# Optimization experiments

Hardware: AMD Instinct MI355X
Metric: run time of the kernel (lower is better)

Reference implementation:

```python
import jax, jax.numpy as jnp
import numpy as np

MODEL_DIM = 1024
N_HEADS = 16
HEAD_DIM = 64  # q_dim == k_dim == v_dim


def setup_inputs() -> dict:
    key = jax.random.key(0)
    ks = jax.random.split(key, 7)
    B, S = 4, 2048
    scale = 1.0 / np.sqrt(MODEL_DIM)
    return {
        "q": jax.random.normal(ks[0], (B, S, MODEL_DIM), dtype=jnp.float32),
        "k": jax.random.normal(ks[1], (B, S, MODEL_DIM), dtype=jnp.float32),
        "v": jax.random.normal(ks[2], (B, S, MODEL_DIM), dtype=jnp.float32),
        # Linear weights stored as [out, in] like torch; no biases.
        "wq": jax.random.normal(ks[3], (N_HEADS * HEAD_DIM, MODEL_DIM), dtype=jnp.float32) * scale,
        "wk": jax.random.normal(ks[4], (N_HEADS * HEAD_DIM, MODEL_DIM), dtype=jnp.float32) * scale,
        "wv": jax.random.normal(ks[5], (N_HEADS * HEAD_DIM, MODEL_DIM), dtype=jnp.float32) * scale,
        "wo": jax.random.normal(ks[6], (MODEL_DIM, N_HEADS * HEAD_DIM), dtype=jnp.float32) * scale,
    }


def reference(q, k, v, wq, wk, wv, wo):
    B, Sq, _ = q.shape
    Sk = k.shape[1]
    # projections: [B,S,D] @ W^T -> [B,S,H*dh] -> [B,H,S,dh]
    qh = (q @ wq.T).reshape(B, Sq, N_HEADS, HEAD_DIM).transpose(0, 2, 1, 3)
    kh = (k @ wk.T).reshape(B, Sk, N_HEADS, HEAD_DIM).transpose(0, 2, 1, 3)
    vh = (v @ wv.T).reshape(B, Sk, N_HEADS, HEAD_DIM).transpose(0, 2, 1, 3)
    # scores [B,H,Sq,Sk], scaled by sqrt(k_dim)
    scores = jnp.einsum('bhqd,bhkd->bhqk', qh, kh) / jnp.sqrt(jnp.float32(HEAD_DIM))
    attn = jax.nn.softmax(scores, axis=-1)
    ctx = jnp.einsum('bhqk,bhkd->bhqd', attn, vh)  # [B,H,Sq,dh]
    ctx = ctx.transpose(0, 2, 1, 3).reshape(B, Sq, N_HEADS * HEAD_DIM)
    return ctx @ wo.T
```

## Files before the change

### kernel.cpp

```cpp
#include <hip/hip_runtime.h>
#include <cstdint>
#include <cstddef>


typedef _Float16 f16x8 __attribute__((ext_vector_type(8)));
typedef _Float16 f16x4 __attribute__((ext_vector_type(4)));
typedef _Float16 f16x2 __attribute__((ext_vector_type(2)));
typedef __fp16 h16x2 __attribute__((ext_vector_type(2)));
typedef float f32x4 __attribute__((ext_vector_type(4)));
typedef float f32x16 __attribute__((ext_vector_type(16)));
typedef unsigned u32x4 __attribute__((ext_vector_type(4)));
typedef int i32x2 __attribute__((ext_vector_type(2)));

#define LDS_CAST(p) ((__attribute__((address_space(3))) void*)(p))
#define GLB_CAST(p) ((const __attribute__((address_space(1))) void*)(p))

__device__ __forceinline__ void gload_lds16(const void* g, void* l) {
  __builtin_amdgcn_global_load_lds(GLB_CAST(g), LDS_CAST(l), 16, 0, 0);
}

__device__ __forceinline__ float fexp2(float x) {
#if __has_builtin(__builtin_amdgcn_exp2f)
  return __builtin_amdgcn_exp2f(x);
#else
  return exp2f(x);
#endif
}

__device__ __forceinline__ f16x2 pkrtz(float a, float b) {
  h16x2 r = __builtin_amdgcn_cvt_pkrtz(a, b);
  return __builtin_bit_cast(f16x2, r);
}

__device__ __forceinline__ float dot2acc(f16x2 a, float acc) {
#if __has_builtin(__builtin_amdgcn_fdot2)
  const f16x2 one2 = {(_Float16)1.0f, (_Float16)1.0f};
  return __builtin_amdgcn_fdot2(a, one2, acc, false);
#else
  return acc + (float)a[0] + (float)a[1];
#endif
}

__device__ __forceinline__ void pl32swap(unsigned& a, unsigned& b) {
#if __has_builtin(__builtin_amdgcn_permlane32_swap)
  i32x2 r = __builtin_amdgcn_permlane32_swap((int)a, (int)b, false, false);
  a = (unsigned)r[0];
  b = (unsigned)r[1];
#else
  asm("v_permlane32_swap_b32 %0, %1" : "+v"(a), "+v"(b));
#endif
}

__global__ void cvt3_kernel(const float* __restrict__ a,
                            const float* __restrict__ b,
                            const float* __restrict__ c,
                            _Float16* __restrict__ oa, _Float16* __restrict__ ob,
                            _Float16* __restrict__ oc) {
  const float* in = blockIdx.z == 0 ? a : blockIdx.z == 1 ? b : c;
  _Float16* out = blockIdx.z == 0 ? oa : blockIdx.z == 1 ? ob : oc;
  int i = blockIdx.x * 256 + threadIdx.x;
  float4 v = ((const float4*)in)[i];
  f16x4 o = {(_Float16)v.x, (_Float16)v.y, (_Float16)v.z, (_Float16)v.w};
  ((f16x4*)out)[i] = o;
}

__global__ void cvt4_kernel(const float* __restrict__ a,
                            const float* __restrict__ b,
                            const float* __restrict__ c,
                            const float* __restrict__ d,
                            _Float16* __restrict__ oa, _Float16* __restrict__ ob,
                            _Float16* __restrict__ oc, _Float16* __restrict__ od) {
  int z = blockIdx.z;
  const float* in = z == 0 ? a : z == 1 ? b : z == 2 ? c : d;
  _Float16* out = z == 0 ? oa : z == 1 ? ob : z == 2 ? oc : od;
  int i = blockIdx.x * 256 + threadIdx.x;
  float4 v = ((const float4*)in)[i];
  f16x4 o = {(_Float16)v.x, (_Float16)v.y, (_Float16)v.z, (_Float16)v.w};
  ((f16x4*)out)[i] = o;
}

template <int MODE>
__device__ __forceinline__ void gemm_core(const _Float16* __restrict__ A,
                                          const _Float16* __restrict__ W,
                                          void* __restrict__ C, float scale,
                                          _Float16* As, _Float16* Bs) {
  constexpr int K = 1024, N = 1024;
  const int tid = threadIdx.x;
  const int wid = tid >> 6;
  const int lane = tid & 63;
  const int quad = lane >> 4;
  const int l16 = lane & 15;
  const int wm = wid >> 1;
  const int wn = wid & 1;
  const int m0 = blockIdx.y * 128;
  const int n0 = blockIdx.x * 128;

  const _Float16* Ag = A + (size_t)m0 * K;
  const _Float16* Bg = W + (size_t)n0 * K;

  f32x4 acc[4][4];
#pragma unroll
  for (int i = 0; i < 4; i++)
#pragma unroll
    for (int j = 0; j < 4; j++) acc[i][j] = (f32x4){0.f, 0.f, 0.f, 0.f};

  const int lrow = lane >> 2;
  const int lcol = (lane & 3) * 8;

  for (int k0 = 0; k0 < K; k0 += 32) {
#pragma unroll
    for (int i = 0; i < 2; i++) {
      int issue = wid * 2 + i;
      gload_lds16(Ag + (size_t)(issue * 16 + lrow) * K + k0 + lcol,
                  &As[issue * 512]);
      gload_lds16(Bg + (size_t)(issue * 16 + lrow) * K + k0 + lcol,
                  &Bs[issue * 512]);
    }
    __syncthreads();
    f16x8 af[4], bfr[4];
#pragma unroll
    for (int mt = 0; mt < 4; mt++)
      af[mt] = *(const f16x8*)&As[(wm * 64 + mt * 16 + l16) * 32 + quad * 8];
#pragma unroll
    for (int nt = 0; nt < 4; nt++)
      bfr[nt] = *(const f16x8*)&Bs[(wn * 64 + nt * 16 + l16) * 32 + quad * 8];
#pragma unroll
    for (int mt = 0; mt < 4; mt++)
#pragma unroll
      for (int nt = 0; nt < 4; nt++)
        acc[mt][nt] = __builtin_amdgcn_mfma_f32_16x16x32_f16(
            af[mt], bfr[nt], acc[mt][nt], 0, 0, 0);
    __syncthreads();
  }

#pragma unroll
  for (int mt = 0; mt < 4; mt++) {
#pragma unroll
    for (int nt = 0; nt < 4; nt++) {
#pragma unroll
      for (int r = 0; r < 4; r++) {
        int m = m0 + wm * 64 + mt * 16 + quad * 4 + r;
        int n = n0 + wn * 64 + nt * 16 + l16;
        float v = acc[mt][nt][r] * scale;
        if (MODE == 0) {
          ((float*)C)[(size_t)m * N + n] = v;
        } else {
          int b = m >> 11, s = m & 2047;
          int h = n >> 6, dd = n & 63;
          size_t bh = (size_t)(b * 16 + h);
          if (MODE == 1) {
            ((_Float16*)C)[(bh * 2048 + s) * 64 + dd] = (_Float16)v;
          } else if (MODE == 3) {
            int kt2 = s >> 5, l32k = s & 31;
            int s4 = dd >> 4, hi8 = (dd >> 3) & 1, j = dd & 7;
            size_t idx = (bh * 32 + (kt2 >> 1)) * 8192 +
                         (((kt2 & 1) * 4 + s4) * 512) + (hi8 * 32 + l32k) * 8 +
                         j;
            ((_Float16*)C)[idx] = (_Float16)v;
          } else {
            int kt = s >> 6, ks = (s >> 4) & 3, hi8 = (s >> 3) & 1, j = s & 7;
            int dt = dd >> 5, l32v = dd & 31;
            size_t idx = (bh * 32 + kt) * 8192 + 4096 + ((dt * 4 + ks) * 512) +
                         (hi8 * 32 + l32v) * 8 + j;
            ((_Float16*)C)[idx] = (_Float16)v;
          }
        }
      }
    }
  }
}

__global__ __launch_bounds__(256) void gemm_qkv(
    const _Float16* __restrict__ qb, const _Float16* __restrict__ kb,
    const _Float16* __restrict__ vb, const _Float16* __restrict__ wq,
    const _Float16* __restrict__ wk, const _Float16* __restrict__ wv,
    _Float16* __restrict__ Qh, _Float16* __restrict__ KVf) {
  __shared__ _Float16 As[128 * 32];
  __shared__ _Float16 Bs[128 * 32];
  if (blockIdx.z == 0)
    gemm_core<1>(qb, wq, Qh, 0.18033688f, As, Bs);
  else if (blockIdx.z == 1)
    gemm_core<3>(kb, wk, KVf, 1.0f, As, Bs);
  else
    gemm_core<4>(vb, wv, KVf, 1.0f, As, Bs);
}

__global__ __launch_bounds__(256) void gemm_wo(const _Float16* __restrict__ ctx,
                                               const _Float16* __restrict__ wo,
                                               float* __restrict__ out) {
  __shared__ _Float16 As[128 * 32];
  __shared__ _Float16 Bs[128 * 32];
  gemm_core<0>(ctx, wo, out, 1.0f, As, Bs);
}

__global__ __launch_bounds__(256, 3) void attn_kernel(
    const _Float16* __restrict__ Qh, const _Float16* __restrict__ KVf,
    _Float16* __restrict__ ctx) {
  __shared__ _Float16 sKV[3][8192];

  const int qt = blockIdx.x;
  const int bh = blockIdx.y;
  const int tid = threadIdx.x;
  const int wid = tid >> 6;
  const int lane = tid & 63;
  const int l32 = lane & 31;
  const int hi = lane >> 5;

  const _Float16* Qg = Qh + ((size_t)bh * 2048 + qt * 128 + wid * 32) * 64;
  const _Float16* KVb = KVf + (size_t)bh * 262144;

  f16x8 aq[4];
#pragma unroll
  for (int s = 0; s < 4; s++)
    aq[s] = *(const f16x8*)(Qg + (size_t)l32 * 64 + s * 16 + hi * 8);

  f32x16 acc[2];
#pragma unroll
  for (int i = 0; i < 16; i++) {
    acc[0][i] = 0.f;
    acc[1][i] = 0.f;
  }
  float lsA = 0.f, lsB = 0.f;

  auto stage = [&](int buf, int kt) {
    const _Float16* t = KVb + (size_t)kt * 8192;
#pragma unroll
    for (int i = 0; i < 4; i++) {
      int c = wid * 4 + i;
      gload_lds16(t + c * 512 + lane * 8, &sKV[buf][c * 512]);
    }
  };

  stage(0, 0);
  int cur = 0;

  for (int kt = 0; kt < 32; kt++) {
    int nxt = (cur == 2) ? 0 : cur + 1;
    if (kt < 31) {
      stage(nxt, kt + 1);
      asm volatile("s_waitcnt vmcnt(4)" ::: "memory");
    } else {
      asm volatile("s_waitcnt vmcnt(0)" ::: "memory");
    }
    __builtin_amdgcn_s_barrier();
    asm volatile("" ::: "memory");

    const _Float16* Ks = sKV[cur];
    const _Float16* Vs = sKV[cur] + 4096;

    f16x8 kf0[4], kf1[4];
#pragma unroll
    for (int s = 0; s < 4; s++) {
      kf0[s] = *(const f16x8*)&Ks[(0 * 4 + s) * 512 + lane * 8];
      kf1[s] = *(const f16x8*)&Ks[(4 + s) * 512 + lane * 8];
    }

    f32x16 s0, s1;
#pragma unroll
    for (int i = 0; i < 16; i++) {
      s0[i] = 0.f;
      s1[i] = 0.f;
    }
#pragma unroll
    for (int s = 0; s < 4; s++) {
      s0 = __builtin_amdgcn_mfma_f32_32x32x16_f16(kf0[s], aq[s], s0, 0, 0, 0);
      s1 = __builtin_amdgcn_mfma_f32_32x32x16_f16(kf1[s], aq[s], s1, 0, 0, 0);
    }

    f16x8 vf0[4], vf1[4];
#pragma unroll
    for (int g = 0; g < 4; g++) {
      vf0[g] = *(const f16x8*)&Vs[(0 * 4 + g) * 512 + lane * 8];
      vf1[g] = *(const f16x8*)&Vs[(4 + g) * 512 + lane * 8];
    }

    unsigned hw[2][8];
#pragma unroll
    for (int i = 0; i < 8; i++) {
      f16x2 hh = pkrtz(fexp2(s0[2 * i]), fexp2(s0[2 * i + 1]));
      if (i & 1)
        lsB = dot2acc(hh, lsB);
      else
        lsA = dot2acc(hh, lsA);
      hw[0][i] = __builtin_bit_cast(unsigned, hh);
    }
#pragma unroll
    for (int i = 0; i < 8; i++) {
      f16x2 hh = pkrtz(fexp2(s1[2 * i]), fexp2(s1[2 * i + 1]));
      if (i & 1)
        lsB = dot2acc(hh, lsB);
      else
        lsA = dot2acc(hh, lsA);
      hw[1][i] = __builtin_bit_cast(unsigned, hh);
    }

#pragma unroll
    for (int st = 0; st < 2; st++)
#pragma unroll
      for (int kh = 0; kh < 2; kh++) {
        unsigned w0 = hw[st][4 * kh + 0], w2 = hw[st][4 * kh + 2];
        unsigned w1 = hw[st][4 * kh + 1], w3 = hw[st][4 * kh + 3];
        pl32swap(w0, w2);
        pl32swap(w1, w3);
        u32x4 wv4 = {w0, w1, w2, w3};
        f16x8 pfrag = __builtin_bit_cast(f16x8, wv4);
        int g = st * 2 + kh;
        acc[0] = __builtin_amdgcn_mfma_f32_32x32x16_f16(vf0[g], pfrag, acc[0],
                                                        0, 0, 0);
        acc[1] = __builtin_amdgcn_mfma_f32_32x32x16_f16(vf1[g], pfrag, acc[1],
                                                        0, 0, 0);
      }

    cur = nxt;
  }

  float lsum = lsA + lsB;
  float l = lsum + __shfl_xor(lsum, 32);
  float inv = 1.f / l;
  const int b = bh >> 4, h = bh & 15;
  int q = qt * 128 + wid * 32 + l32;
  _Float16* outp = ctx + ((size_t)b * 2048 + q) * 1024 + h * 64;
#pragma unroll
  for (int dt = 0; dt < 2; dt++)
#pragma unroll
    for (int g = 0; g < 4; g++) {
      f16x4 o;
#pragma unroll
      for (int c = 0; c < 4; c++) o[c] = (_Float16)(acc[dt][g * 4 + c] * inv);
      *(f16x4*)(outp + dt * 32 + g * 8 + hi * 4) = o;
    }
}

extern "C" void kernel_launch(void* const* d_in, const int* in_sizes, int n_in,
                              void* d_out, int out_size, void* d_ws,
                              size_t ws_size, hipStream_t stream) {
  const float* q = (const float*)d_in[0];
  const float* k = (const float*)d_in[1];
  const float* v = (const float*)d_in[2];
  const float* wq = (const float*)d_in[3];
  const float* wk = (const float*)d_in[4];
  const float* wv = (const float*)d_in[5];
  const float* wo = (const float*)d_in[6];
  float* out = (float*)d_out;

  const size_t SD = (size_t)8192 * 1024;
  const size_t WSZ = (size_t)1024 * 1024;

  _Float16* ws = (_Float16*)d_ws;
  _Float16* qb = ws;
  _Float16* kb = ws + 1 * SD;
  _Float16* vb = ws + 2 * SD;
  _Float16* Qh = ws + 3 * SD;
  _Float16* KVf = ws + 4 * SD;
  _Float16* ctx = ws + 6 * SD;
  _Float16* wqb = ws + 7 * SD;
  _Float16* wkb = wqb + WSZ;
  _Float16* wvb = wqb + 2 * WSZ;
  _Float16* wob = wqb + 3 * WSZ;

  cvt3_kernel<<<dim3(8192, 1, 3), 256, 0, stream>>>(q, k, v, qb, kb, vb);
  cvt4_kernel<<<dim3(1024, 1, 4), 256, 0, stream>>>(wq, wk, wv, wo, wqb, wkb,
                                                    wvb, wob);

  gemm_qkv<<<dim3(8, 64, 3), 256, 0, stream>>>(qb, kb, vb, wqb, wkb, wvb, Qh,
                                               KVf);

  attn_kernel<<<dim3(16, 64), 256, 0, stream>>>(Qh, KVf, ctx);

  gemm_wo<<<dim3(8, 64), 256, 0, stream>>>(ctx, wob, out);
}
```

Measured before the change: 334.6 us.

## Triple-buffer GEMM LDS loads with swizzle, block remap, and merged convert kernel

The GEMM main loop becomes a 3-stage LDS ring. Global-to-LDS loads for tile t+2 are issued before computing tile t, using explicit vmcnt waits and a single barrier per iteration in place of two __syncthreads. LDS columns are XOR-swizzled to reduce bank conflicts on the fragment reads. Block indices are remapped so that neighbouring blocks share weight tiles, and the two fp32→fp16 conversion kernels are merged into one launch. LDS use per GEMM block triples, and correctness depends on the hand-written waitcnt counts matching the number of loads in flight.

```diff
diff --git a/kernel.cpp b/kernel.cpp
--- a/kernel.cpp
+++ b/kernel.cpp
@@ -51,31 +51,32 @@
 #endif
 }
 
-__global__ void cvt3_kernel(const float* __restrict__ a,
-                            const float* __restrict__ b,
-                            const float* __restrict__ c,
-                            _Float16* __restrict__ oa, _Float16* __restrict__ ob,
-                            _Float16* __restrict__ oc) {
-  const float* in = blockIdx.z == 0 ? a : blockIdx.z == 1 ? b : c;
-  _Float16* out = blockIdx.z == 0 ? oa : blockIdx.z == 1 ? ob : oc;
-  int i = blockIdx.x * 256 + threadIdx.x;
-  float4 v = ((const float4*)in)[i];
-  f16x4 o = {(_Float16)v.x, (_Float16)v.y, (_Float16)v.z, (_Float16)v.w};
-  ((f16x4*)out)[i] = o;
-}
-
-__global__ void cvt4_kernel(const float* __restrict__ a,
-                            const float* __restrict__ b,
-                            const float* __restrict__ c,
-                            const float* __restrict__ d,
-                            _Float16* __restrict__ oa, _Float16* __restrict__ ob,
-                            _Float16* __restrict__ oc, _Float16* __restrict__ od) {
-  int z = blockIdx.z;
-  const float* in = z == 0 ? a : z == 1 ? b : z == 2 ? c : d;
-  _Float16* out = z == 0 ? oa : z == 1 ? ob : z == 2 ? oc : od;
-  int i = blockIdx.x * 256 + threadIdx.x;
-  float4 v = ((const float4*)in)[i];
-  f16x4 o = {(_Float16)v.x, (_Float16)v.y, (_Float16)v.z, (_Float16)v.w};
+__global__ void cvt_all(const float* __restrict__ q, const float* __restrict__ k,
+                        const float* __restrict__ v, const float* __restrict__ wq,
+                        const float* __restrict__ wk, const float* __restrict__ wv,
+                        const float* __restrict__ wo, _Float16* __restrict__ oq,
+                        _Float16* __restrict__ ok, _Float16* __restrict__ ov,
+                        _Float16* __restrict__ owq, _Float16* __restrict__ owk,
+                        _Float16* __restrict__ owv, _Float16* __restrict__ owo) {
+  int id = blockIdx.x;
+  const float* in;
+  _Float16* out;
+  int base;
+  if (id < 24576) {
+    int z = id >> 13;
+    base = (id & 8191) * 256;
+    in = z == 0 ? q : z == 1 ? k : v;
+    out = z == 0 ? oq : z == 1 ? ok : ov;
+  } else {
+    int id2 = id - 24576;
+    int z = id2 >> 10;
+    base = (id2 & 1023) * 256;
+    in = z == 0 ? wq : z == 1 ? wk : z == 2 ? wv : wo;
+    out = z == 0 ? owq : z == 1 ? owk : z == 2 ? owv : owo;
+  }
+  int i = base + threadIdx.x;
+  float4 vv = ((const float4*)in)[i];
+  f16x4 o = {(_Float16)vv.x, (_Float16)vv.y, (_Float16)vv.z, (_Float16)vv.w};
   ((f16x4*)out)[i] = o;
 }
 
@@ -92,8 +93,11 @@
   const int l16 = lane & 15;
   const int wm = wid >> 1;
   const int wn = wid & 1;
-  const int m0 = blockIdx.y * 128;
-  const int n0 = blockIdx.x * 128;
+
+  int lin = blockIdx.y * 8 + blockIdx.x;
+  int swz = (lin & 7) * 64 + (lin >> 3);
+  const int m0 = (swz >> 3) * 128;
+  const int n0 = (swz & 7) * 128;
 
   const _Float16* Ag = A + (size_t)m0 * K;
   const _Float16* Bg = W + (size_t)n0 * K;
@@ -105,32 +109,56 @@
     for (int j = 0; j < 4; j++) acc[i][j] = (f32x4){0.f, 0.f, 0.f, 0.f};
 
   const int lrow = lane >> 2;
-  const int lcol = (lane & 3) * 8;
-
-  for (int k0 = 0; k0 < K; k0 += 32) {
+  const int swsrc = ((lane & 3) ^ ((lane >> 3) & 3)) * 8;
+
+  auto stage = [&](int buf, int k0) {
 #pragma unroll
     for (int i = 0; i < 2; i++) {
       int issue = wid * 2 + i;
-      gload_lds16(Ag + (size_t)(issue * 16 + lrow) * K + k0 + lcol,
-                  &As[issue * 512]);
-      gload_lds16(Bg + (size_t)(issue * 16 + lrow) * K + k0 + lcol,
-                  &Bs[issue * 512]);
-    }
-    __syncthreads();
+      gload_lds16(Ag + (size_t)(issue * 16 + lrow) * K + k0 + swsrc,
+                  &As[buf * 4096 + issue * 512]);
+      gload_lds16(Bg + (size_t)(issue * 16 + lrow) * K + k0 + swsrc,
+                  &Bs[buf * 4096 + issue * 512]);
+    }
+  };
+
+  stage(0, 0);
+  stage(1, 32);
+
+  const int swq = (quad ^ ((l16 >> 1) & 3)) * 8;
+  int rb = 0;
+
+  for (int t = 0; t < 32; t++) {
+    if (t < 31)
+      asm volatile("s_waitcnt vmcnt(4)" ::: "memory");
+    else
+      asm volatile("s_waitcnt vmcnt(0)" ::: "memory");
+    __builtin_amdgcn_s_barrier();
+    asm volatile("" ::: "memory");
+
+    if (t < 30) {
+      int sb = rb + 2;
+      if (sb >= 3) sb -= 3;
+      stage(sb, (t + 2) * 32);
+    }
+
+    const _Float16* Ab = &As[rb * 4096];
+    const _Float16* Bb = &Bs[rb * 4096];
     f16x8 af[4], bfr[4];
 #pragma unroll
     for (int mt = 0; mt < 4; mt++)
-      af[mt] = *(const f16x8*)&As[(wm * 64 + mt * 16 + l16) * 32 + quad * 8];
+      af[mt] = *(const f16x8*)&Ab[(wm * 64 + mt * 16 + l16) * 32 + swq];
 #pragma unroll
     for (int nt = 0; nt < 4; nt++)
-      bfr[nt] = *(const f16x8*)&Bs[(wn * 64 + nt * 16 + l16) * 32 + quad * 8];
+      bfr[nt] = *(const f16x8*)&Bb[(wn * 64 + nt * 16 + l16) * 32 + swq];
 #pragma unroll
     for (int mt = 0; mt < 4; mt++)
 #pragma unroll
       for (int nt = 0; nt < 4; nt++)
         acc[mt][nt] = __builtin_amdgcn_mfma_f32_16x16x32_f16(
             af[mt], bfr[nt], acc[mt][nt], 0, 0, 0);
-    __syncthreads();
+
+    rb = (rb == 2) ? 0 : rb + 1;
   }
 
 #pragma unroll
@@ -175,8 +203,8 @@
     const _Float16* __restrict__ vb, const _Float16* __restrict__ wq,
     const _Float16* __restrict__ wk, const _Float16* __restrict__ wv,
     _Float16* __restrict__ Qh, _Float16* __restrict__ KVf) {
-  __shared__ _Float16 As[128 * 32];
-  __shared__ _Float16 Bs[128 * 32];
+  __shared__ _Float16 As[3 * 128 * 32];
+  __shared__ _Float16 Bs[3 * 128 * 32];
   if (blockIdx.z == 0)
     gemm_core<1>(qb, wq, Qh, 0.18033688f, As, Bs);
   else if (blockIdx.z == 1)
@@ -188,8 +216,8 @@
 __global__ __launch_bounds__(256) void gemm_wo(const _Float16* __restrict__ ctx,
                                                const _Float16* __restrict__ wo,
                                                float* __restrict__ out) {
-  __shared__ _Float16 As[128 * 32];
-  __shared__ _Float16 Bs[128 * 32];
+  __shared__ _Float16 As[3 * 128 * 32];
+  __shared__ _Float16 Bs[3 * 128 * 32];
   gemm_core<0>(ctx, wo, out, 1.0f, As, Bs);
 }
 
@@ -358,9 +386,8 @@
   _Float16* wvb = wqb + 2 * WSZ;
   _Float16* wob = wqb + 3 * WSZ;
 
-  cvt3_kernel<<<dim3(8192, 1, 3), 256, 0, stream>>>(q, k, v, qb, kb, vb);
-  cvt4_kernel<<<dim3(1024, 1, 4), 256, 0, stream>>>(wq, wk, wv, wo, wqb, wkb,
-                                                    wvb, wob);
+  cvt_all<<<dim3(28672), 256, 0, stream>>>(q, k, v, wq, wk, wv, wo, qb, kb, vb,
+                                           wqb, wkb, wvb, wob);
 
   gemm_qkv<<<dim3(8, 64, 3), 256, 0, stream>>>(qb, kb, vb, wqb, wkb, wvb, Qh,
                                                KVf);
```

Result: slower. 342.9 us (+2.5%).
